# Performance work log

Measured on AMD Instinct MI355X. Metric: run time of the kernel, lower is better.

Reference implementation:

```python
import jax, jax.numpy as jnp
import numpy as np

HEIGHT = 256
WIDTH = 256
SIGMAINV = 7000.0  # DIB-R style soft-silhouette sharpness
EPS = 1e-10


def setup_inputs():
    key = jax.random.key(0)
    k1, k2, k3, k4, k5 = jax.random.split(key, 5)
    B, P, F = 1, 160, 256
    TH = TW = 1024
    points_bxpx3 = 0.8 * jax.random.normal(k1, (B, P, 3), jnp.float32)
    faces_fx3 = jax.random.randint(k2, (F, 3), 0, P)
    camera_rot_bx3x3 = jnp.broadcast_to(jnp.eye(3, dtype=jnp.float32), (B, 3, 3))
    camera_pos_bx3 = jnp.tile(jnp.array([[0.0, 0.0, 2.5]], jnp.float32), (B, 1))
    camera_proj_3x1 = jnp.array([[2.5], [2.5], [-1.0]], jnp.float32)
    uv_bxpx2 = jax.random.uniform(k3, (B, P, 2), jnp.float32)
    ft_fx3 = jax.random.randint(k4, (F, 3), 0, P)
    texture_bx3xthxtw = jax.random.uniform(k5, (B, 3, TH, TW), jnp.float32)
    return {"points_bxpx3": points_bxpx3, "faces_fx3": faces_fx3,
            "camera_rot_bx3x3": camera_rot_bx3x3, "camera_pos_bx3": camera_pos_bx3,
            "camera_proj_3x1": camera_proj_3x1, "uv_bxpx2": uv_bxpx2,
            "ft_fx3": ft_fx3, "texture_bx3xthxtw": texture_bx3xthxtw}


def _perspective(points_bxpx3, faces_fx3, cam_rot, cam_pos, cam_proj):
    p = points_bxpx3 - cam_pos[:, None, :]
    p = jnp.einsum('bpj,bij->bpi', p, cam_rot)                  # camera frame [B,P,3]
    xy3 = p * cam_proj.reshape(1, 1, 3)
    xy = xy3[..., :2] / xy3[..., 2:3]                           # projected 2D [B,P,2]
    pf0 = p[:, faces_fx3[:, 0]]
    pf1 = p[:, faces_fx3[:, 1]]
    pf2 = p[:, faces_fx3[:, 2]]
    points3d_bxfx9 = jnp.concatenate([pf0, pf1, pf2], axis=2)
    points2d_bxfx6 = jnp.concatenate([xy[:, faces_fx3[:, 0]], xy[:, faces_fx3[:, 1]], xy[:, faces_fx3[:, 2]]], axis=2)
    normal_bxfx3 = jnp.cross(pf1 - pf0, pf2 - pf0)
    return points3d_bxfx9, points2d_bxfx6, normal_bxfx3


def _edge_dist2(px, py, ax, ay, bx, by):
    ex, ey = bx - ax, by - ay
    t = jnp.clip(((px - ax) * ex + (py - ay) * ey) / (ex * ex + ey * ey + EPS), 0.0, 1.0)
    dx, dy = px - (ax + t * ex), py - (ay + t * ey)
    return dx * dx + dy * dy


def _rasterize(points3d_bxfx9, points2d_bxfx6, normalz_bxfx1, feat_bxfx9, H, W):
    B, F, _ = points2d_bxfx6.shape
    x0, y0, x1, y1, x2, y2 = [points2d_bxfx6[:, None, :, i] for i in range(6)]   # [B,1,F]
    xs = (jnp.arange(W, dtype=jnp.float32) + 0.5) / W * 2.0 - 1.0
    ys = 1.0 - (jnp.arange(H, dtype=jnp.float32) + 0.5) / H * 2.0
    px = jnp.tile(xs[None, :], (H, 1)).reshape(1, -1, 1)                          # [1,N,1]
    py = jnp.tile(ys[:, None], (1, W)).reshape(1, -1, 1)
    A = (x1 - x0) * (y2 - y0) - (x2 - x0) * (y1 - y0)
    invA = jnp.where(jnp.abs(A) > EPS, 1.0 / jnp.where(jnp.abs(A) > EPS, A, 1.0), 0.0)
    w0 = ((x1 - px) * (y2 - py) - (x2 - px) * (y1 - py)) * invA                   # [B,N,F]
    w1 = ((x2 - px) * (y0 - py) - (x0 - px) * (y2 - py)) * invA
    w2 = 1.0 - w0 - w1
    valid = (jnp.abs(A) > EPS) & (normalz_bxfx1[:, None, :, 0] > 0)               # backface cull
    inside = (w0 >= 0) & (w1 >= 0) & (w2 >= 0) & valid
    z0 = points3d_bxfx9[:, None, :, 2]
    z1 = points3d_bxfx9[:, None, :, 5]
    z2 = points3d_bxfx9[:, None, :, 8]
    z = w0 * z0 + w1 * z1 + w2 * z2                                               # camera looks down -z
    fid = jnp.argmax(jnp.where(inside, z, -1e10), axis=2)                          # nearest covering face
    hit = jnp.any(inside, axis=2)
    take = lambda a: jnp.take_along_axis(a, fid[:, :, None], axis=2)[:, :, 0]
    w0s, w1s, w2s = take(w0), take(w1), take(w2)
    fverts = feat_bxfx9.reshape(B, F, 3, 3)
    fsel = jax.vmap(lambda fv, ii: fv[ii])(fverts, fid)                            # [B,N,3verts,3feat]
    imfeat = (w0s[..., None] * fsel[:, :, 0] + w1s[..., None] * fsel[:, :, 1] + w2s[..., None] * fsel[:, :, 2])
    imfeat = imfeat * hit[..., None].astype(imfeat.dtype)
    # soft silhouette probability (DIB-R): 1 - prod_f (1 - exp(-d^2 * sigmainv))
    d2 = jnp.minimum(_edge_dist2(px, py, x0, y0, x1, y1),
                     jnp.minimum(_edge_dist2(px, py, x1, y1, x2, y2),
                                 _edge_dist2(px, py, x2, y2, x0, y0)))
    d2 = jnp.where(inside, 0.0, d2)
    log_miss = jnp.log(jnp.clip(1.0 - jnp.exp(-d2 * SIGMAINV), 1e-10, 1.0))
    improb = 1.0 - jnp.exp(jnp.sum(jnp.where(valid, log_miss, 0.0), axis=2))
    return imfeat.reshape(B, H, W, 3), improb.reshape(B, H, W, 1)


def _fragmentshader(imtexcoord_bxhxwx2, texture_bx3xthxtw, hardmask_bxhxwx1):
    th, tw = texture_bx3xthxtw.shape[2], texture_bx3xthxtw.shape[3]
    x = imtexcoord_bxhxwx2[..., 0] * (tw - 1)
    y = (1.0 - imtexcoord_bxhxwx2[..., 1]) * (th - 1)
    x0f = jnp.clip(jnp.floor(x), 0, tw - 1)
    y0f = jnp.clip(jnp.floor(y), 0, th - 1)
    x0 = x0f.astype(jnp.int32)
    y0 = y0f.astype(jnp.int32)
    x1 = jnp.clip(x0 + 1, 0, tw - 1)
    y1 = jnp.clip(y0 + 1, 0, th - 1)
    wx = jnp.clip(x - x0f, 0.0, 1.0)[..., None]
    wy = jnp.clip(y - y0f, 0.0, 1.0)[..., None]
    tex = texture_bx3xthxtw.transpose(0, 2, 3, 1)                                 # [B,th,tw,3]
    g = jax.vmap(lambda t, yy, xx: t[yy, xx])
    c00, c01 = g(tex, y0, x0), g(tex, y0, x1)
    c10, c11 = g(tex, y1, x0), g(tex, y1, x1)
    color = (c00 * (1 - wx) + c01 * wx) * (1 - wy) + (c10 * (1 - wx) + c11 * wx) * wy
    return jnp.clip(color * hardmask_bxhxwx1, 0.0, 1.0)


def reference(points_bxpx3, faces_fx3, camera_rot_bx3x3, camera_pos_bx3, camera_proj_3x1, uv_bxpx2, ft_fx3, texture_bx3xthxtw):
    points3d, points2d, normal = _perspective(points_bxpx3, faces_fx3, camera_rot_bx3x3, camera_pos_bx3, camera_proj_3x1)
    normalz = normal[:, :, 2:3]
    normal1 = normal / (jnp.sqrt(jnp.sum(normal * normal, axis=2, keepdims=True)) + EPS)
    c0 = uv_bxpx2[:, ft_fx3[:, 0]]
    c1 = uv_bxpx2[:, ft_fx3[:, 1]]
    c2 = uv_bxpx2[:, ft_fx3[:, 2]]
    mask = jnp.ones_like(c0[:, :, :1])
    uv_bxfx9 = jnp.concatenate([c0, mask, c1, mask, c2, mask], axis=2)
    imfeat, improb = _rasterize(points3d, points2d, normalz, uv_bxfx9, HEIGHT, WIDTH)
    imrender = _fragmentshader(imfeat[..., :2], texture_bx3xthxtw, imfeat[..., 2:3])
    return imrender, improb, normal1
```

## Files before the change

### kernel.cpp

```cpp
#include <hip/hip_runtime.h>
#include <math.h>

#define HGT 256
#define WID 256
#define NF 256
#define NP 160
#define SIGMAINV 7000.0f
#define EPSF 1e-10f
#define TW 1024
#define TH 1024
#define CHUNKS 8
#define FPC 32
#define PPB 32
#define CUT2 3.29e-3f

struct FaceGeo {
    float x0, y0, x1, y1, x2, y2;
    float z0, z1, z2;
    float invA;
    float bminx, bminy, bmaxx, bmaxy;
    int   valid;
    int   pad;
};
struct FaceUV { float u0, v0, u1, v1, u2, v2; };

__device__ __forceinline__ float mul_opaque(float a, float b)
{
    float r;
    asm volatile("v_mul_f32 %0, %1, %2" : "=v"(r) : "v"(a), "v"(b));
    return r;
}
__device__ __forceinline__ float fma_opaque(float a, float b, float c)
{
    float r;
    asm volatile("v_fma_f32 %0, %1, %2, %3" : "=v"(r) : "v"(a), "v"(b), "v"(c));
    return r;
}

__global__ __launch_bounds__(256) void prep_kernel(
    const float* __restrict__ pts,
    const int*   __restrict__ faces,
    const float* __restrict__ rot,
    const float* __restrict__ cpos,
    const float* __restrict__ proj,
    const float* __restrict__ uvs,
    const int*   __restrict__ ft,
    FaceGeo*     __restrict__ fg,
    FaceUV*      __restrict__ fuv,
    float*       __restrict__ out_normal)
{
    __shared__ float sp[NP][3];
    __shared__ float sxy[NP][2];
    const int t = threadIdx.x;

    const float r00 = rot[0], r01 = rot[1], r02 = rot[2];
    const float r10 = rot[3], r11 = rot[4], r12 = rot[5];
    const float r20 = rot[6], r21 = rot[7], r22 = rot[8];
    const float cx = cpos[0], cy = cpos[1], cz = cpos[2];
    const float p0 = proj[0], p1 = proj[1], p2 = proj[2];

    if (t < NP) {
        float ax = pts[t * 3 + 0] - cx;
        float ay = pts[t * 3 + 1] - cy;
        float az = pts[t * 3 + 2] - cz;
        float qx = r00 * ax + r01 * ay + r02 * az;
        float qy = r10 * ax + r11 * ay + r12 * az;
        float qz = r20 * ax + r21 * ay + r22 * az;
        sp[t][0] = qx; sp[t][1] = qy; sp[t][2] = qz;
        float zz = qz * p2;
        sxy[t][0] = (qx * p0) / zz;
        sxy[t][1] = (qy * p1) / zz;
    }
    __syncthreads();

    if (t < NF) {
        int i0 = faces[t * 3 + 0], i1 = faces[t * 3 + 1], i2 = faces[t * 3 + 2];
        float ax = sp[i0][0], ay = sp[i0][1], az = sp[i0][2];
        float bx = sp[i1][0], by = sp[i1][1], bz = sp[i1][2];
        float gx = sp[i2][0], gy = sp[i2][1], gz = sp[i2][2];

        float e1x = bx - ax, e1y = by - ay, e1z = bz - az;
        float e2x = gx - ax, e2y = gy - ay, e2z = gz - az;
        float tnx = mul_opaque(e1z, e2y);
        float nx  = fma_opaque(e1y, e2z, -tnx);
        float tny = mul_opaque(e1x, e2z);
        float ny  = fma_opaque(e1z, e2x, -tny);
        float tnz = mul_opaque(e1y, e2x);
        float nz  = fma_opaque(e1x, e2y, -tnz);
        float s   = (mul_opaque(nx, nx) + mul_opaque(ny, ny)) + mul_opaque(nz, nz);
        float nl  = sqrtf(s) + 1e-10f;
        out_normal[t * 3 + 0] = nx / nl;
        out_normal[t * 3 + 1] = ny / nl;
        out_normal[t * 3 + 2] = nz / nl;

        FaceGeo f;
        f.x0 = sxy[i0][0]; f.y0 = sxy[i0][1];
        f.x1 = sxy[i1][0]; f.y1 = sxy[i1][1];
        f.x2 = sxy[i2][0]; f.y2 = sxy[i2][1];
        f.z0 = az; f.z1 = bz; f.z2 = gz;
        float A = mul_opaque(f.x1 - f.x0, f.y2 - f.y0)
                - mul_opaque(f.x2 - f.x0, f.y1 - f.y0);
        bool okA = fabsf(A) > EPSF;
        f.invA  = okA ? 1.0f / A : 0.0f;
        f.valid = (okA && nz > 0.0f) ? 1 : 0;
        f.bminx = fminf(fminf(f.x0, f.x1), f.x2);
        f.bminy = fminf(fminf(f.y0, f.y1), f.y2);
        f.bmaxx = fmaxf(fmaxf(f.x0, f.x1), f.x2);
        f.bmaxy = fmaxf(fmaxf(f.y0, f.y1), f.y2);
        f.pad = 0;
        fg[t] = f;

        int j0 = ft[t * 3 + 0], j1 = ft[t * 3 + 1], j2 = ft[t * 3 + 2];
        FaceUV u;
        u.u0 = uvs[j0 * 2]; u.v0 = uvs[j0 * 2 + 1];
        u.u1 = uvs[j1 * 2]; u.v1 = uvs[j1 * 2 + 1];
        u.u2 = uvs[j2 * 2]; u.v2 = uvs[j2 * 2 + 1];
        fuv[t] = u;
    }
}

__device__ __forceinline__ float edge_d2(float px, float py, float ax, float ay,
                                         float bx, float by)
{
    float ex = bx - ax, ey = by - ay;
    float t = ((px - ax) * ex + (py - ay) * ey) / (ex * ex + ey * ey + EPSF);
    t = fminf(fmaxf(t, 0.0f), 1.0f);
    float dx = px - (ax + t * ex);
    float dy = py - (ay + t * ey);
    return dx * dx + dy * dy;
}

__global__ __launch_bounds__(256) void raster_kernel(
    const FaceGeo* __restrict__ fg,
    const FaceUV*  __restrict__ fuv,
    const float*   __restrict__ tex,
    float*         __restrict__ out)
{
    __shared__ float4 sgeo4[NF * 4];
    __shared__ float  sZ[256];
    __shared__ int    sFid[256];
    __shared__ float  sLog[256];

    const int t = threadIdx.x;
    {
        const float4* src4 = (const float4*)fg;
        #pragma unroll
        for (int i = 0; i < 4; ++i)
            sgeo4[t + i * 256] = src4[t + i * 256];
    }
    __syncthreads();
    const FaceGeo* sf = (const FaceGeo*)sgeo4;

    const int chunk = t >> 5;
    const int p     = t & 31;
    const int tx = (blockIdx.x & 31) * 8;
    const int ty = (blockIdx.x >> 5) * 4;
    {
        const int w = tx + (p & 7);
        const int h = ty + (p >> 3);
        const float px = ((float)w + 0.5f) / (float)WID * 2.0f - 1.0f;
        const float py = 1.0f - ((float)h + 0.5f) / (float)HGT * 2.0f;

        float best_z = -1e30f;
        int   fid = 0;
        float logsum = 0.0f;

        const int f0 = chunk * FPC;
        for (int f = f0; f < f0 + FPC; ++f) {
            const FaceGeo& fc = sf[f];
            if (!fc.valid) continue;
            float ddx = fmaxf(fmaxf(fc.bminx - px, px - fc.bmaxx), 0.0f);
            float ddy = fmaxf(fmaxf(fc.bminy - py, py - fc.bmaxy), 0.0f);
            if (ddx * ddx + ddy * ddy > CUT2) continue;

            float ax = fc.x1 - px, ay = fc.y1 - py;
            float bx = fc.x2 - px, by = fc.y2 - py;
            float gx = fc.x0 - px, gy = fc.y0 - py;
            float w0 = (ax * by - bx * ay) * fc.invA;
            float w1 = (bx * gy - gx * by) * fc.invA;
            float w2 = 1.0f - w0 - w1;
            bool inside = (w0 >= 0.0f) & (w1 >= 0.0f) & (w2 >= 0.0f);
            if (inside) {
                float z = w0 * fc.z0 + w1 * fc.z1 + w2 * fc.z2;
                if (z > best_z) { best_z = z; fid = f; }
                logsum += -23.025850929940457f;
            } else {
                float d2 = edge_d2(px, py, fc.x0, fc.y0, fc.x1, fc.y1);
                d2 = fminf(d2, edge_d2(px, py, fc.x1, fc.y1, fc.x2, fc.y2));
                d2 = fminf(d2, edge_d2(px, py, fc.x2, fc.y2, fc.x0, fc.y0));
                float a = d2 * SIGMAINV;
                if (a < 23.03f) {
                    float e = __expf(-a);
                    logsum += __logf(fmaxf(1.0f - e, 1e-10f));
                }
            }
        }
        sZ[t] = best_z; sFid[t] = fid; sLog[t] = logsum;
    }
    __syncthreads();

    if (t < PPB) {
        float bz = -1e30f; int bf = 0; float ls = 0.0f;
        #pragma unroll
        for (int c = 0; c < CHUNKS; ++c) {
            int i = c * PPB + t;
            ls += sLog[i];
            float z = sZ[i];
            if (z > bz) { bz = z; bf = sFid[i]; }
        }
        bool hit = bz > -1e29f;

        const int w = tx + (t & 7);
        const int h = ty + (t >> 3);
        const int pix = h * WID + w;
        out[HGT * WID * 3 + pix] = 1.0f - __expf(ls);

        float cr = 0.0f, cg = 0.0f, cb = 0.0f;
        if (hit) {
            const float px = ((float)w + 0.5f) / (float)WID * 2.0f - 1.0f;
            const float py = 1.0f - ((float)h + 0.5f) / (float)HGT * 2.0f;
            const FaceGeo& fc = sf[bf];
            float axx = fc.x1 - px, ayy = fc.y1 - py;
            float bxx = fc.x2 - px, byy = fc.y2 - py;
            float gxx = fc.x0 - px, gyy = fc.y0 - py;
            float w0 = (axx * byy - bxx * ayy) * fc.invA;
            float w1 = (bxx * gyy - gxx * byy) * fc.invA;
            float w2 = 1.0f - w0 - w1;
            FaceUV uv = fuv[bf];
            float u = w0 * uv.u0 + w1 * uv.u1 + w2 * uv.u2;
            float v = w0 * uv.v0 + w1 * uv.v1 + w2 * uv.v2;
            float mask = w0 + w1 + w2;

            float x = u * (float)(TW - 1);
            float y = (1.0f - v) * (float)(TH - 1);
            float x0f = fminf(fmaxf(floorf(x), 0.0f), (float)(TW - 1));
            float y0f = fminf(fmaxf(floorf(y), 0.0f), (float)(TH - 1));
            int xi0 = (int)x0f, yi0 = (int)y0f;
            int xi1 = min(xi0 + 1, TW - 1);
            int yi1 = min(yi0 + 1, TH - 1);
            float wx = fminf(fmaxf(x - x0f, 0.0f), 1.0f);
            float wy = fminf(fmaxf(y - y0f, 0.0f), 1.0f);

            int o00 = yi0 * TW + xi0, o01 = yi0 * TW + xi1;
            int o10 = yi1 * TW + xi0, o11 = yi1 * TW + xi1;
            #pragma unroll
            for (int c = 0; c < 3; ++c) {
                const float* tp = tex + c * (TW * TH);
                float c00 = tp[o00], c01 = tp[o01], c10 = tp[o10], c11 = tp[o11];
                float col = (c00 * (1.0f - wx) + c01 * wx) * (1.0f - wy)
                          + (c10 * (1.0f - wx) + c11 * wx) * wy;
                col = fminf(fmaxf(col * mask, 0.0f), 1.0f);
                if (c == 0) cr = col; else if (c == 1) cg = col; else cb = col;
            }
        }
        out[pix * 3 + 0] = cr;
        out[pix * 3 + 1] = cg;
        out[pix * 3 + 2] = cb;
    }
}

extern "C" void kernel_launch(void* const* d_in, const int* in_sizes, int n_in,
                              void* d_out, int out_size, void* d_ws, size_t ws_size,
                              hipStream_t stream)
{
    const float* pts   = (const float*)d_in[0];
    const int*   faces = (const int*)  d_in[1];
    const float* rot   = (const float*)d_in[2];
    const float* cpos  = (const float*)d_in[3];
    const float* proj  = (const float*)d_in[4];
    const float* uvs   = (const float*)d_in[5];
    const int*   ft    = (const int*)  d_in[6];
    const float* tex   = (const float*)d_in[7];
    float* out = (float*)d_out;

    FaceGeo* fg  = (FaceGeo*)d_ws;
    FaceUV*  fuv = (FaceUV*)((char*)d_ws + NF * sizeof(FaceGeo));

    prep_kernel<<<1, 256, 0, stream>>>(pts, faces, rot, cpos, proj, uvs, ft,
                                       fg, fuv, out + HGT * WID * 3 + HGT * WID);
    raster_kernel<<<(HGT * WID) / PPB, 256, 0, stream>>>(fg, fuv, tex, out);
}
```

Before: 99.48 us.

## Fuse face preparation into raster kernel, recomputing geometry per block

```diff
diff --git a/kernel.cpp b/kernel.cpp
--- a/kernel.cpp
+++ b/kernel.cpp
@@ -22,7 +22,6 @@
     int   valid;
     int   pad;
 };
-struct FaceUV { float u0, v0, u1, v1, u2, v2; };
 
 __device__ __forceinline__ float mul_opaque(float a, float b)
 {
@@ -37,7 +36,18 @@
     return r;
 }
 
-__global__ __launch_bounds__(256) void prep_kernel(
+__device__ __forceinline__ float edge_d2(float px, float py, float ax, float ay,
+                                         float bx, float by)
+{
+    float ex = bx - ax, ey = by - ay;
+    float t = ((px - ax) * ex + (py - ay) * ey) / (ex * ex + ey * ey + EPSF);
+    t = fminf(fmaxf(t, 0.0f), 1.0f);
+    float dx = px - (ax + t * ex);
+    float dy = py - (ay + t * ey);
+    return dx * dx + dy * dy;
+}
+
+__global__ __launch_bounds__(256) void render_fused(
     const float* __restrict__ pts,
     const int*   __restrict__ faces,
     const float* __restrict__ rot,
@@ -45,12 +55,19 @@
     const float* __restrict__ proj,
     const float* __restrict__ uvs,
     const int*   __restrict__ ft,
-    FaceGeo*     __restrict__ fg,
-    FaceUV*      __restrict__ fuv,
-    float*       __restrict__ out_normal)
-{
-    __shared__ float sp[NP][3];
-    __shared__ float sxy[NP][2];
+    const float* __restrict__ tex,
+    float*       __restrict__ out)
+{
+    __shared__ float4 sgeo4[NF * 4];
+    __shared__ float  scratch[800];
+
+    FaceGeo* sf  = (FaceGeo*)sgeo4;
+    float*   sp  = scratch;
+    float*   sxy = scratch + 480;
+    float*   sZ   = scratch;
+    float*   sLog = scratch + 256;
+    int*     sFid = (int*)(scratch + 512);
+
     const int t = threadIdx.x;
 
     const float r00 = rot[0], r01 = rot[1], r02 = rot[2];
@@ -66,18 +83,18 @@
         float qx = r00 * ax + r01 * ay + r02 * az;
         float qy = r10 * ax + r11 * ay + r12 * az;
         float qz = r20 * ax + r21 * ay + r22 * az;
-        sp[t][0] = qx; sp[t][1] = qy; sp[t][2] = qz;
+        sp[t * 3 + 0] = qx; sp[t * 3 + 1] = qy; sp[t * 3 + 2] = qz;
         float zz = qz * p2;
-        sxy[t][0] = (qx * p0) / zz;
-        sxy[t][1] = (qy * p1) / zz;
+        sxy[t * 2 + 0] = (qx * p0) / zz;
+        sxy[t * 2 + 1] = (qy * p1) / zz;
     }
     __syncthreads();
 
-    if (t < NF) {
+    {
         int i0 = faces[t * 3 + 0], i1 = faces[t * 3 + 1], i2 = faces[t * 3 + 2];
-        float ax = sp[i0][0], ay = sp[i0][1], az = sp[i0][2];
-        float bx = sp[i1][0], by = sp[i1][1], bz = sp[i1][2];
-        float gx = sp[i2][0], gy = sp[i2][1], gz = sp[i2][2];
+        float ax = sp[i0 * 3 + 0], ay = sp[i0 * 3 + 1], az = sp[i0 * 3 + 2];
+        float bx = sp[i1 * 3 + 0], by = sp[i1 * 3 + 1], bz = sp[i1 * 3 + 2];
+        float gx = sp[i2 * 3 + 0], gy = sp[i2 * 3 + 1], gz = sp[i2 * 3 + 2];
 
         float e1x = bx - ax, e1y = by - ay, e1z = bz - az;
         float e2x = gx - ax, e2y = gy - ay, e2z = gz - az;
@@ -87,16 +104,19 @@
         float ny  = fma_opaque(e1z, e2x, -tny);
         float tnz = mul_opaque(e1y, e2x);
         float nz  = fma_opaque(e1x, e2y, -tnz);
-        float s   = (mul_opaque(nx, nx) + mul_opaque(ny, ny)) + mul_opaque(nz, nz);
-        float nl  = sqrtf(s) + 1e-10f;
-        out_normal[t * 3 + 0] = nx / nl;
-        out_normal[t * 3 + 1] = ny / nl;
-        out_normal[t * 3 + 2] = nz / nl;
+        if (blockIdx.x == 0) {
+            float s  = (mul_opaque(nx, nx) + mul_opaque(ny, ny)) + mul_opaque(nz, nz);
+            float nl = sqrtf(s) + 1e-10f;
+            float* out_normal = out + HGT * WID * 3 + HGT * WID;
+            out_normal[t * 3 + 0] = nx / nl;
+            out_normal[t * 3 + 1] = ny / nl;
+            out_normal[t * 3 + 2] = nz / nl;
+        }
 
         FaceGeo f;
-        f.x0 = sxy[i0][0]; f.y0 = sxy[i0][1];
-        f.x1 = sxy[i1][0]; f.y1 = sxy[i1][1];
-        f.x2 = sxy[i2][0]; f.y2 = sxy[i2][1];
+        f.x0 = sxy[i0 * 2 + 0]; f.y0 = sxy[i0 * 2 + 1];
+        f.x1 = sxy[i1 * 2 + 0]; f.y1 = sxy[i1 * 2 + 1];
+        f.x2 = sxy[i2 * 2 + 0]; f.y2 = sxy[i2 * 2 + 1];
         f.z0 = az; f.z1 = bz; f.z2 = gz;
         float A = mul_opaque(f.x1 - f.x0, f.y2 - f.y0)
                 - mul_opaque(f.x2 - f.x0, f.y1 - f.y0);
@@ -108,48 +128,9 @@
         f.bmaxx = fmaxf(fmaxf(f.x0, f.x1), f.x2);
         f.bmaxy = fmaxf(fmaxf(f.y0, f.y1), f.y2);
         f.pad = 0;
-        fg[t] = f;
-
-        int j0 = ft[t * 3 + 0], j1 = ft[t * 3 + 1], j2 = ft[t * 3 + 2];
-        FaceUV u;
-        u.u0 = uvs[j0 * 2]; u.v0 = uvs[j0 * 2 + 1];
-        u.u1 = uvs[j1 * 2]; u.v1 = uvs[j1 * 2 + 1];
-        u.u2 = uvs[j2 * 2]; u.v2 = uvs[j2 * 2 + 1];
-        fuv[t] = u;
-    }
-}
-
-__device__ __forceinline__ float edge_d2(float px, float py, float ax, float ay,
-                                         float bx, float by)
-{
-    float ex = bx - ax, ey = by - ay;
-    float t = ((px - ax) * ex + (py - ay) * ey) / (ex * ex + ey * ey + EPSF);
-    t = fminf(fmaxf(t, 0.0f), 1.0f);
-    float dx = px - (ax + t * ex);
-    float dy = py - (ay + t * ey);
-    return dx * dx + dy * dy;
-}
-
-__global__ __launch_bounds__(256) void raster_kernel(
-    const FaceGeo* __restrict__ fg,
-    const FaceUV*  __restrict__ fuv,
-    const float*   __restrict__ tex,
-    float*         __restrict__ out)
-{
-    __shared__ float4 sgeo4[NF * 4];
-    __shared__ float  sZ[256];
-    __shared__ int    sFid[256];
-    __shared__ float  sLog[256];
-
-    const int t = threadIdx.x;
-    {
-        const float4* src4 = (const float4*)fg;
-        #pragma unroll
-        for (int i = 0; i < 4; ++i)
-            sgeo4[t + i * 256] = src4[t + i * 256];
+        sf[t] = f;
     }
     __syncthreads();
-    const FaceGeo* sf = (const FaceGeo*)sgeo4;
 
     const int chunk = t >> 5;
     const int p     = t & 31;
@@ -226,9 +207,9 @@
             float w0 = (axx * byy - bxx * ayy) * fc.invA;
             float w1 = (bxx * gyy - gxx * byy) * fc.invA;
             float w2 = 1.0f - w0 - w1;
-            FaceUV uv = fuv[bf];
-            float u = w0 * uv.u0 + w1 * uv.u1 + w2 * uv.u2;
-            float v = w0 * uv.v0 + w1 * uv.v1 + w2 * uv.v2;
+            int j0 = ft[bf * 3 + 0], j1 = ft[bf * 3 + 1], j2 = ft[bf * 3 + 2];
+            float u = w0 * uvs[j0 * 2 + 0] + w1 * uvs[j1 * 2 + 0] + w2 * uvs[j2 * 2 + 0];
+            float v = w0 * uvs[j0 * 2 + 1] + w1 * uvs[j1 * 2 + 1] + w2 * uvs[j2 * 2 + 1];
             float mask = w0 + w1 + w2;
 
             float x = u * (float)(TW - 1);
@@ -273,10 +254,6 @@
     const float* tex   = (const float*)d_in[7];
     float* out = (float*)d_out;
 
-    FaceGeo* fg  = (FaceGeo*)d_ws;
-    FaceUV*  fuv = (FaceUV*)((char*)d_ws + NF * sizeof(FaceGeo));
-
-    prep_kernel<<<1, 256, 0, stream>>>(pts, faces, rot, cpos, proj, uvs, ft,
-                                       fg, fuv, out + HGT * WID * 3 + HGT * WID);
-    raster_kernel<<<(HGT * WID) / PPB, 256, 0, stream>>>(fg, fuv, tex, out);
-}
+    render_fused<<<(HGT * WID) / PPB, 256, 0, stream>>>(
+        pts, faces, rot, cpos, proj, uvs, ft, tex, out);
+}
```

Measured after the change: 98.56 us. Within noise of the previous version (-0.9%).
